# Optimization experiments

Measured on AMD Instinct MI355X. Metric: run time of the kernel, lower is better.

The kernel has to match this reference:

```python
import jax, jax.numpy as jnp
import numpy as np

TEMPERATURE = 0.1
B, S, D, V = 4, 256, 768, 50257


def setup_inputs() -> dict:
    key = jax.random.key(0)
    k1, k2 = jax.random.split(key)
    return {
        "pred_embeds": jax.random.normal(k1, (B, S, D), dtype=jnp.float32),
        "embed_weight": jax.random.normal(k2, (V, D), dtype=jnp.float32),
    }


def reference(pred_embeds, embed_weight):
    # metric == 'l2': scores = -||p - t||^2, computed via the GEMM identity
    # -(||p||^2 + ||t||^2 - 2 p.t) instead of a (B,S,V,D) broadcast diff.
    p_sq = jnp.sum(pred_embeds * pred_embeds, axis=-1)        # (B,S)
    t_sq = jnp.sum(embed_weight * embed_weight, axis=-1)      # (V,)
    dot = jnp.einsum('bsd,vd->bsv', pred_embeds, embed_weight)  # (B,S,V)
    scores = 2.0 * dot - p_sq[..., None] - t_sq               # (B,S,V)

    softmax_pred_probs = jax.nn.softmax(scores / TEMPERATURE, axis=-1)
    predictions = jnp.argmax(softmax_pred_probs, axis=-1)      # (B,S) int

    # straight-through one-hot over probs
    y_hard = jax.nn.one_hot(predictions, V, dtype=softmax_pred_probs.dtype)
    pred_probs = y_hard - jax.lax.stop_gradient(softmax_pred_probs) + softmax_pred_probs

    # straight-through embedding lookup
    n_pred_embs = embed_weight[predictions]                    # (B,S,D)
    pred_embeds_st = pred_embeds + jax.lax.stop_gradient(n_pred_embs - pred_embeds)

    return (pred_embeds_st, pred_embeds, predictions, pred_probs, softmax_pred_probs)
```

## Files before the change

kernel.cpp:

```cpp
#include <hip/hip_runtime.h>
#include <math.h>

namespace {

constexpr int Bb = 4, Ss = 256, Dd = 768, Vv = 50257;
constexpr int Mm = Bb * Ss;
constexpr int BM = 128, BN = 128, BK = 32;
constexpr int NS = Dd / BK;
constexpr int TW = (Vv + BN - 1) / BN;
constexpr int TA = Mm / BM;
constexpr int CHUNK = BM * BK;
constexpr float SC = 14.4269504088896341f;

typedef _Float16 f16x8 __attribute__((ext_vector_type(8)));
typedef float f32x4 __attribute__((ext_vector_type(4)));

constexpr size_t WPLANE = (size_t)TW * NS * CHUNK;
constexpr size_t APLANE = (size_t)TA * NS * CHUNK;

__device__ __forceinline__ void gload_lds16(const void* g, void* l) {
    typedef __attribute__((address_space(3))) void lds_t;
    typedef const __attribute__((address_space(1))) void gm_t;
    __builtin_amdgcn_global_load_lds((gm_t*)g, (lds_t*)l, 16, 0, 0);
}

__global__ __launch_bounds__(256) void tsq_kernel(const float* __restrict__ W,
                                                  float* __restrict__ tsq) {
    int gid  = blockIdx.x * blockDim.x + threadIdx.x;
    int wave = gid >> 6;
    int lane = threadIdx.x & 63;
    if (wave >= Vv) return;
    const float4* row = reinterpret_cast<const float4*>(W + (size_t)wave * Dd);
    float s = 0.f;
#pragma unroll
    for (int i = 0; i < 3; ++i) {
        float4 v = row[lane + 64 * i];
        s = fmaf(v.x, v.x, s);
        s = fmaf(v.y, v.y, s);
        s = fmaf(v.z, v.z, s);
        s = fmaf(v.w, v.w, s);
    }
#pragma unroll
    for (int off = 32; off > 0; off >>= 1) s += __shfl_down(s, off);
    if (lane == 0) tsq[wave] = s;
}

__global__ __launch_bounds__(256) void convert_pack(const float* __restrict__ src,
                                                    _Float16* __restrict__ hp,
                                                    _Float16* __restrict__ lp,
                                                    int nrows) {
    const int t    = blockIdx.x;
    const int wid  = threadIdx.x >> 6;
    const int lane = threadIdx.x & 63;
    const int u    = blockIdx.y * 4 + wid;
    const int s    = u >> 1;
    const int half = u & 1;
    const int r    = half * 64 + lane;
    const int v    = t * BM + r;

    float vals[32];
    if (v < nrows) {
        const float4* p = reinterpret_cast<const float4*>(src + (size_t)v * Dd + s * BK);
#pragma unroll
        for (int i = 0; i < 8; ++i) *reinterpret_cast<float4*>(&vals[4 * i]) = p[i];
    } else {
#pragma unroll
        for (int i = 0; i < 32; ++i) vals[i] = 0.f;
    }
    const size_t chunk = ((size_t)t * NS + s) * CHUNK;
#pragma unroll
    for (int fq = 0; fq < 4; ++fq) {
        _Float16 hi[8], lo[8];
#pragma unroll
        for (int e = 0; e < 8; ++e) {
            const float x = vals[fq * 8 + e];
            const _Float16 h = (_Float16)x;
            hi[e] = h;
            lo[e] = (_Float16)(x - (float)h);
        }
        *reinterpret_cast<f16x8*>(&hp[chunk + fq * (BM * 8) + (size_t)r * 8]) =
            *reinterpret_cast<const f16x8*>(hi);
        *reinterpret_cast<f16x8*>(&lp[chunk + fq * (BM * 8) + (size_t)r * 8]) =
            *reinterpret_cast<const f16x8*>(lo);
    }
}

__global__ __launch_bounds__(256) void gemm_kernel(const _Float16* __restrict__ Ahp,
                                                   const _Float16* __restrict__ Alp,
                                                   const _Float16* __restrict__ Whp,
                                                   const _Float16* __restrict__ Wlp,
                                                   const float* __restrict__ tsq,
                                                   float* __restrict__ scores) {
    __shared__ _Float16 lds[4][CHUNK];

    const int tid  = threadIdx.x;
    const int wid  = tid >> 6;
    const int lane = tid & 63;
    const int wr   = wid >> 1;
    const int wc   = wid & 1;
    const int fr   = lane & 15;
    const int fq   = lane >> 4;
    const int tn   = blockIdx.x;
    const int tm   = blockIdx.y;

    const _Float16* gA_h = Ahp + (size_t)tm * NS * CHUNK;
    const _Float16* gA_l = Alp + (size_t)tm * NS * CHUNK;
    const _Float16* gW_h = Whp + (size_t)tn * NS * CHUNK;
    const _Float16* gW_l = Wlp + (size_t)tn * NS * CHUNK;

    f32x4 acc[4][4];
#pragma unroll
    for (int m = 0; m < 4; ++m)
#pragma unroll
        for (int n = 0; n < 4; ++n) acc[m][n] = (f32x4){0.f, 0.f, 0.f, 0.f};

    for (int s = 0; s < NS; ++s) {
        if (s) __syncthreads();
        const size_t so = (size_t)s * CHUNK;
        const _Float16* gsrc[4] = {gA_h + so, gA_l + so, gW_h + so, gW_l + so};
#pragma unroll
        for (int c = 0; c < 4; ++c) {
#pragma unroll
            for (int i = 0; i < 2; ++i) {
                const int seg = wid * 2 + i;
                gload_lds16(gsrc[c] + seg * 512 + lane * 8, &lds[c][seg * 512]);
            }
        }
        __syncthreads();

        f16x8 ah[4], al[4];
#pragma unroll
        for (int m = 0; m < 4; ++m) {
            const int r = wr * 64 + m * 16 + fr;
            ah[m] = *reinterpret_cast<const f16x8*>(&lds[0][fq * (BM * 8) + r * 8]);
            al[m] = *reinterpret_cast<const f16x8*>(&lds[1][fq * (BM * 8) + r * 8]);
        }
#pragma unroll
        for (int n = 0; n < 4; ++n) {
            const int c = wc * 64 + n * 16 + fr;
            const f16x8 wh = *reinterpret_cast<const f16x8*>(&lds[2][fq * (BM * 8) + c * 8]);
            const f16x8 wl = *reinterpret_cast<const f16x8*>(&lds[3][fq * (BM * 8) + c * 8]);
#pragma unroll
            for (int m = 0; m < 4; ++m) {
                acc[m][n] = __builtin_amdgcn_mfma_f32_16x16x32_f16(ah[m], wh, acc[m][n], 0, 0, 0);
                acc[m][n] = __builtin_amdgcn_mfma_f32_16x16x32_f16(al[m], wh, acc[m][n], 0, 0, 0);
                acc[m][n] = __builtin_amdgcn_mfma_f32_16x16x32_f16(ah[m], wl, acc[m][n], 0, 0, 0);
            }
        }
    }

#pragma unroll
    for (int n = 0; n < 4; ++n) {
        const int gn = tn * BN + wc * 64 + n * 16 + fr;
        if (gn >= Vv) continue;
        const float t = tsq[gn];
#pragma unroll
        for (int m = 0; m < 4; ++m) {
            const int gm = tm * BM + wr * 64 + m * 16 + fq * 4;
#pragma unroll
            for (int r = 0; r < 4; ++r) {
                scores[(size_t)(gm + r) * Vv + gn] = fmaf(2.f, acc[m][n][r], -t);
            }
        }
    }
}

__global__ __launch_bounds__(256) void finalize_kernel(const float* __restrict__ A,
                                                       const float* __restrict__ W,
                                                       float* __restrict__ out0,
                                                       float* __restrict__ out1,
                                                       float* __restrict__ out2,
                                                       float* __restrict__ out3,
                                                       float* __restrict__ out4) {
    const int row = blockIdx.x;
    const int tid = threadIdx.x;
    float* srow = out4 + (size_t)row * Vv;
    float* hrow = out3 + (size_t)row * Vv;
    constexpr int NV4 = Vv >> 2;

    const float4* s4 = reinterpret_cast<const float4*>(srow);

    float m = -INFINITY;
    int   idx = 0;
    float sum = 0.f;
    for (int i = tid; i < NV4; i += 256) {
        const float4 v = s4[i];
        const float vv[4] = {v.x, v.y, v.z, v.w};
#pragma unroll
        for (int j = 0; j < 4; ++j) {
            const float val = vv[j];
            if (val > m) {
                sum *= exp2f((m - val) * SC);
                m = val;
                idx = 4 * i + j;
            }
            sum += exp2f((val - m) * SC);
        }
    }
    if (tid == 0) {
        const float val = srow[Vv - 1];
        if (val > m) { sum *= exp2f((m - val) * SC); m = val; idx = Vv - 1; }
        sum += exp2f((val - m) * SC);
    }

    __shared__ float smax[256];
    __shared__ int   sidx[256];
    __shared__ float ssum[256];
    smax[tid] = m; sidx[tid] = idx; ssum[tid] = sum;
    __syncthreads();
#pragma unroll
    for (int off = 128; off > 0; off >>= 1) {
        if (tid < off) {
            const float m1 = smax[tid], m2 = smax[tid + off];
            const int   i1 = sidx[tid], i2 = sidx[tid + off];
            const float s1 = ssum[tid], s2 = ssum[tid + off];
            if (m2 > m1 || (m2 == m1 && i2 < i1)) {
                smax[tid] = m2; sidx[tid] = i2;
                ssum[tid] = s1 * exp2f((m1 - m2) * SC) + s2;
            } else {
                ssum[tid] = s1 + s2 * exp2f((m2 - m1) * SC);
            }
        }
        __syncthreads();
    }
    const float gmax = smax[0];
    const int   pred = sidx[0];
    const float inv  = 1.0f / ssum[0];
    __syncthreads();

    float4* p4 = reinterpret_cast<float4*>(srow);
    float4* h4 = reinterpret_cast<float4*>(hrow);
    for (int i = tid; i < NV4; i += 256) {
        const float4 v = s4[i];
        const int b = 4 * i;
        float4 p, h;
        p.x = exp2f((v.x - gmax) * SC) * inv;
        p.y = exp2f((v.y - gmax) * SC) * inv;
        p.z = exp2f((v.z - gmax) * SC) * inv;
        p.w = exp2f((v.w - gmax) * SC) * inv;
        h.x = (b + 0 == pred) ? 1.f : 0.f;
        h.y = (b + 1 == pred) ? 1.f : 0.f;
        h.z = (b + 2 == pred) ? 1.f : 0.f;
        h.w = (b + 3 == pred) ? 1.f : 0.f;
        p4[i] = p;
        h4[i] = h;
    }
    if (tid == 0) {
        const float val = srow[Vv - 1];
        srow[Vv - 1] = exp2f((val - gmax) * SC) * inv;
        hrow[Vv - 1] = (pred == Vv - 1) ? 1.f : 0.f;
        out2[row] = (float)pred;
    }

    const float4* wrow = reinterpret_cast<const float4*>(W + (size_t)pred * Dd);
    const float4* arow = reinterpret_cast<const float4*>(A + (size_t)row * Dd);
    float4* o0 = reinterpret_cast<float4*>(out0 + (size_t)row * Dd);
    float4* o1 = reinterpret_cast<float4*>(out1 + (size_t)row * Dd);
    if (tid < Dd / 4) {
        o0[tid] = wrow[tid];
        o1[tid] = arow[tid];
    }
}

}

extern "C" void kernel_launch(void* const* d_in, const int* in_sizes, int n_in,
                              void* d_out, int out_size, void* d_ws, size_t ws_size,
                              hipStream_t stream) {
    const float* pred_embeds  = (const float*)d_in[0];
    const float* embed_weight = (const float*)d_in[1];

    float* out  = (float*)d_out;
    float* out0 = out;
    float* out1 = out0 + (size_t)Mm * Dd;
    float* out2 = out1 + (size_t)Mm * Dd;
    float* out3 = out2 + Mm;
    float* out4 = out3 + (size_t)Mm * Vv;

    _Float16* Whp = (_Float16*)out3;
    _Float16* Wlp = Whp + WPLANE;
    _Float16* Ahp = Wlp + WPLANE;
    _Float16* Alp = Ahp + APLANE;
    float*    tsq = (float*)(Alp + APLANE);

    tsq_kernel<<<(Vv + 3) / 4, 256, 0, stream>>>(embed_weight, tsq);
    convert_pack<<<dim3(TW, 12), 256, 0, stream>>>(embed_weight, Whp, Wlp, Vv);
    convert_pack<<<dim3(TA, 12), 256, 0, stream>>>(pred_embeds, Ahp, Alp, Mm);

    gemm_kernel<<<dim3(TW, TA), 256, 0, stream>>>(Ahp, Alp, Whp, Wlp, tsq, out4);

    finalize_kernel<<<Mm, 256, 0, stream>>>(pred_embeds, embed_weight,
                                            out0, out1, out2, out3, out4);
}
```

Measured before the change: 549.6 us.

## Fuse row-norm into convert-pack, remap GEMM blocks per XCD, split softmax chains

Merges the separate weight row-norm kernel into the fp16 hi/lo conversion kernel, so the weight matrix is read once instead of twice. It also computes unused norms for the activation rows. The GEMM now uses a flat 1D grid, remapped so each XCD handles a contiguous range of W tiles across all M tiles, to improve L2 reuse of W. The finalize online-softmax loop keeps four independent max/sum chains to shorten dependency chains, then merges them. This adds some bookkeeping, and the new conversion thread mapping may coalesce global reads less well.

```diff
diff --git a/kernel.cpp b/kernel.cpp
--- a/kernel.cpp
+++ b/kernel.cpp
@@ -24,65 +24,52 @@
     __builtin_amdgcn_global_load_lds((gm_t*)g, (lds_t*)l, 16, 0, 0);
 }
 
-__global__ __launch_bounds__(256) void tsq_kernel(const float* __restrict__ W,
-                                                  float* __restrict__ tsq) {
-    int gid  = blockIdx.x * blockDim.x + threadIdx.x;
-    int wave = gid >> 6;
-    int lane = threadIdx.x & 63;
-    if (wave >= Vv) return;
-    const float4* row = reinterpret_cast<const float4*>(W + (size_t)wave * Dd);
-    float s = 0.f;
-#pragma unroll
-    for (int i = 0; i < 3; ++i) {
-        float4 v = row[lane + 64 * i];
-        s = fmaf(v.x, v.x, s);
-        s = fmaf(v.y, v.y, s);
-        s = fmaf(v.z, v.z, s);
-        s = fmaf(v.w, v.w, s);
-    }
-#pragma unroll
-    for (int off = 32; off > 0; off >>= 1) s += __shfl_down(s, off);
-    if (lane == 0) tsq[wave] = s;
-}
-
-__global__ __launch_bounds__(256) void convert_pack(const float* __restrict__ src,
-                                                    _Float16* __restrict__ hp,
-                                                    _Float16* __restrict__ lp,
-                                                    int nrows) {
-    const int t    = blockIdx.x;
-    const int wid  = threadIdx.x >> 6;
-    const int lane = threadIdx.x & 63;
-    const int u    = blockIdx.y * 4 + wid;
-    const int s    = u >> 1;
-    const int half = u & 1;
-    const int r    = half * 64 + lane;
-    const int v    = t * BM + r;
-
-    float vals[32];
-    if (v < nrows) {
-        const float4* p = reinterpret_cast<const float4*>(src + (size_t)v * Dd + s * BK);
-#pragma unroll
-        for (int i = 0; i < 8; ++i) *reinterpret_cast<float4*>(&vals[4 * i]) = p[i];
-    } else {
-#pragma unroll
-        for (int i = 0; i < 32; ++i) vals[i] = 0.f;
-    }
-    const size_t chunk = ((size_t)t * NS + s) * CHUNK;
-#pragma unroll
-    for (int fq = 0; fq < 4; ++fq) {
-        _Float16 hi[8], lo[8];
-#pragma unroll
-        for (int e = 0; e < 8; ++e) {
-            const float x = vals[fq * 8 + e];
-            const _Float16 h = (_Float16)x;
-            hi[e] = h;
-            lo[e] = (_Float16)(x - (float)h);
-        }
-        *reinterpret_cast<f16x8*>(&hp[chunk + fq * (BM * 8) + (size_t)r * 8]) =
-            *reinterpret_cast<const f16x8*>(hi);
-        *reinterpret_cast<f16x8*>(&lp[chunk + fq * (BM * 8) + (size_t)r * 8]) =
-            *reinterpret_cast<const f16x8*>(lo);
-    }
+__global__ __launch_bounds__(256) void convert_pack_tsq(const float* __restrict__ src,
+                                                        _Float16* __restrict__ hp,
+                                                        _Float16* __restrict__ lp,
+                                                        float* __restrict__ sumsq,
+                                                        int nrows) {
+    const int t   = blockIdx.x;
+    const int tid = threadIdx.x;
+    const int r   = blockIdx.y * 64 + (tid >> 2);
+    const int q   = tid & 3;
+    const int v   = t * BM + r;
+    const bool valid = v < nrows;
+
+    float sq = 0.f;
+#pragma unroll
+    for (int i = 0; i < 6; ++i) {
+        const int s = q * 6 + i;
+        float vals[32];
+        if (valid) {
+            const float4* p = reinterpret_cast<const float4*>(src + (size_t)v * Dd + s * BK);
+#pragma unroll
+            for (int k = 0; k < 8; ++k) *reinterpret_cast<float4*>(&vals[4 * k]) = p[k];
+        } else {
+#pragma unroll
+            for (int k = 0; k < 32; ++k) vals[k] = 0.f;
+        }
+        const size_t chunk = ((size_t)t * NS + s) * CHUNK;
+#pragma unroll
+        for (int fq = 0; fq < 4; ++fq) {
+            _Float16 hi[8], lo[8];
+#pragma unroll
+            for (int e = 0; e < 8; ++e) {
+                const float x = vals[fq * 8 + e];
+                sq = fmaf(x, x, sq);
+                const _Float16 h = (_Float16)x;
+                hi[e] = h;
+                lo[e] = (_Float16)(x - (float)h);
+            }
+            *reinterpret_cast<f16x8*>(&hp[chunk + fq * (BM * 8) + (size_t)r * 8]) =
+                *reinterpret_cast<const f16x8*>(hi);
+            *reinterpret_cast<f16x8*>(&lp[chunk + fq * (BM * 8) + (size_t)r * 8]) =
+                *reinterpret_cast<const f16x8*>(lo);
+        }
+    }
+    sq += __shfl_xor(sq, 1);
+    sq += __shfl_xor(sq, 2);
+    if (valid && q == 0) sumsq[v] = sq;
 }
 
 __global__ __launch_bounds__(256) void gemm_kernel(const _Float16* __restrict__ Ahp,
@@ -93,6 +80,13 @@
                                                    float* __restrict__ scores) {
     __shared__ _Float16 lds[4][CHUNK];
 
+    const int b    = blockIdx.x;
+    const int xcd  = b & 7;
+    const int slot = b >> 3;
+    const int tn   = xcd * 50 + (slot >> 3);
+    const int tm   = slot & 7;
+    if (tn >= TW) return;
+
     const int tid  = threadIdx.x;
     const int wid  = tid >> 6;
     const int lane = tid & 63;
@@ -100,8 +94,6 @@
     const int wc   = wid & 1;
     const int fr   = lane & 15;
     const int fq   = lane >> 4;
-    const int tn   = blockIdx.x;
-    const int tm   = blockIdx.y;
 
     const _Float16* gA_h = Ahp + (size_t)tm * NS * CHUNK;
     const _Float16* gA_l = Alp + (size_t)tm * NS * CHUNK;
@@ -180,21 +172,34 @@
 
     const float4* s4 = reinterpret_cast<const float4*>(srow);
 
-    float m = -INFINITY;
-    int   idx = 0;
-    float sum = 0.f;
+    float m4[4]  = {-INFINITY, -INFINITY, -INFINITY, -INFINITY};
+    int   id4[4] = {0, 0, 0, 0};
+    float sm4[4] = {0.f, 0.f, 0.f, 0.f};
     for (int i = tid; i < NV4; i += 256) {
         const float4 v = s4[i];
         const float vv[4] = {v.x, v.y, v.z, v.w};
 #pragma unroll
         for (int j = 0; j < 4; ++j) {
             const float val = vv[j];
-            if (val > m) {
-                sum *= exp2f((m - val) * SC);
-                m = val;
-                idx = 4 * i + j;
-            }
-            sum += exp2f((val - m) * SC);
+            if (val > m4[j]) {
+                sm4[j] *= exp2f((m4[j] - val) * SC);
+                m4[j] = val;
+                id4[j] = 4 * i + j;
+            }
+            sm4[j] += exp2f((val - m4[j]) * SC);
+        }
+    }
+    float m = m4[0];
+    int   idx = id4[0];
+    float sum = sm4[0];
+#pragma unroll
+    for (int j = 1; j < 4; ++j) {
+        if (m4[j] > m || (m4[j] == m && id4[j] < idx)) {
+            sum = sum * exp2f((m - m4[j]) * SC) + sm4[j];
+            m = m4[j];
+            idx = id4[j];
+        } else {
+            sum += sm4[j] * exp2f((m4[j] - m) * SC);
         }
     }
     if (tid == 0) {
@@ -282,12 +287,12 @@
     _Float16* Ahp = Wlp + WPLANE;
     _Float16* Alp = Ahp + APLANE;
     float*    tsq = (float*)(Alp + APLANE);
-
-    tsq_kernel<<<(Vv + 3) / 4, 256, 0, stream>>>(embed_weight, tsq);
-    convert_pack<<<dim3(TW, 12), 256, 0, stream>>>(embed_weight, Whp, Wlp, Vv);
-    convert_pack<<<dim3(TA, 12), 256, 0, stream>>>(pred_embeds, Ahp, Alp, Mm);
-
-    gemm_kernel<<<dim3(TW, TA), 256, 0, stream>>>(Ahp, Alp, Whp, Wlp, tsq, out4);
+    float*    asq = tsq + Vv;
+
+    convert_pack_tsq<<<dim3(TW, 2), 256, 0, stream>>>(embed_weight, Whp, Wlp, tsq, Vv);
+    convert_pack_tsq<<<dim3(TA, 2), 256, 0, stream>>>(pred_embeds, Ahp, Alp, asq, Mm);
+
+    gemm_kernel<<<3200, 256, 0, stream>>>(Ahp, Alp, Whp, Wlp, tsq, out4);
 
     finalize_kernel<<<Mm, 256, 0, stream>>>(pred_embeds, embed_weight,
                                             out0, out1, out2, out3, out4);
```

After: 519.0 us. 5.6% less time.
